# Kernel tuning notes

Measured on AMD Instinct MI355X. Metric: run time of the kernel, lower is better.

The kernel has to match this reference:

```python
import jax, jax.numpy as jnp
import numpy as np

NUM_HEADS = 32      # query heads
NUM_KV_HEADS = 8    # GQA kv heads
HEAD_DIM = 128
BS = 16             # decode batch (one new token per sequence)
KV_LEN = 2048       # pages (page_size=1 -> tokens) per sequence
NUM_SLOTS = BS * KV_LEN
SCALE = HEAD_DIM ** -0.5


def setup_inputs() -> dict:
    key = jax.random.key(0)
    ks = jax.random.split(key, 6)
    q = jax.random.normal(ks[0], (BS, NUM_HEADS * HEAD_DIM), dtype=jnp.float32)
    k = jax.random.normal(ks[1], (BS, NUM_KV_HEADS * HEAD_DIM), dtype=jnp.float32)
    v = jax.random.normal(ks[2], (BS, NUM_KV_HEADS * HEAD_DIM), dtype=jnp.float32)
    k_cache = jax.random.normal(ks[3], (NUM_SLOTS, NUM_KV_HEADS * HEAD_DIM), dtype=jnp.float32)
    v_cache = jax.random.normal(ks[4], (NUM_SLOTS, NUM_KV_HEADS * HEAD_DIM), dtype=jnp.float32)
    # paged layout: each sequence owns KV_LEN non-contiguous slots (page_size=1)
    perm = jax.random.permutation(ks[5], NUM_SLOTS).astype(jnp.int32)
    page_indices = perm.reshape(BS, KV_LEN)            # [BS, KV_LEN] slot ids
    slot_mapping = page_indices[:, -1]                 # new token written to last page
    return {"q": q, "k": k, "v": v, "k_cache": k_cache, "v_cache": v_cache,
            "slot_mapping": slot_mapping, "page_indices": page_indices}


def reference(q, k, v, k_cache, v_cache, slot_mapping, page_indices):
    # store_kvcache: scatter new K/V rows into flat [num_slots, Hkv*d] caches
    k_cache = k_cache.at[slot_mapping].set(k)
    v_cache = v_cache.at[slot_mapping].set(v)
    # paged gather (page_size=1): [BS, KV_LEN, Hkv, d]
    keys = k_cache[page_indices].reshape(BS, KV_LEN, NUM_KV_HEADS, HEAD_DIM)
    vals = v_cache[page_indices].reshape(BS, KV_LEN, NUM_KV_HEADS, HEAD_DIM)
    # GQA: query head h uses kv head h // group
    group = NUM_HEADS // NUM_KV_HEADS
    qh = q.reshape(BS, NUM_KV_HEADS, group, HEAD_DIM)
    scores = jnp.einsum('bhgd,blhd->bhgl', qh, keys) * SCALE   # [BS,Hkv,g,L]
    p = jax.nn.softmax(scores, axis=-1)
    o = jnp.einsum('bhgl,blhd->bhgd', p, vals)                 # [BS,Hkv,g,d]
    return o.reshape(BS, NUM_HEADS * HEAD_DIM)
```

## Files before the change

### kernel.cpp

```cpp
#include <hip/hip_runtime.h>
#include <math.h>

constexpr int NUM_HEADS    = 32;
constexpr int NUM_KV_HEADS = 8;
constexpr int HEAD_DIM     = 128;
constexpr int BS           = 16;
constexpr int KV_LEN       = 2048;
constexpr int GROUP        = NUM_HEADS / NUM_KV_HEADS;
constexpr int NCHUNK       = 16;
constexpr int CHUNK        = KV_LEN / NCHUNK;
constexpr int NIT          = CHUNK / 16;

__device__ __forceinline__ void dma16(const float* g, float* l) {
    __builtin_amdgcn_global_load_lds(
        (const __attribute__((address_space(1))) void*)g,
        (__attribute__((address_space(3))) void*)l,
        16, 0, 0);
}

__global__ __launch_bounds__(256, 4) void attn_partial_kernel(
    const float* __restrict__ q,
    const float* __restrict__ knew,
    const float* __restrict__ vnew,
    const float* __restrict__ k_cache,
    const float* __restrict__ v_cache,
    const int*   __restrict__ page_indices,
    float* __restrict__ ws_o,
    float* __restrict__ ws_m,
    float* __restrict__ ws_s)
{
    const int bid   = blockIdx.x;
    const int chunk = bid % NCHUNK;
    const int h     = (bid / NCHUNK) % NUM_KV_HEADS;
    const int b     = bid / (NCHUNK * NUM_KV_HEADS);

    const int tid  = threadIdx.x;
    const int wid  = tid >> 6;
    const int lane = tid & 63;
    const int g    = lane >> 4;
    const int sub  = lane & 15;
    const int lg   = wid * 4 + g;

    const int lbase = chunk * CHUNK;

    __shared__ float smem[2][4][1024];

    const float qscale = 0.08838834764831845f * 1.4426950408889634f;

    float qv[GROUP][8];
#pragma unroll
    for (int hg = 0; hg < GROUP; ++hg) {
        const float* qp = q + ((size_t)b * NUM_HEADS + h * GROUP + hg) * HEAD_DIM;
        const float4 a = *(const float4*)(qp + sub * 4);
        const float4 c = *(const float4*)(qp + 64 + sub * 4);
        qv[hg][0] = a.x * qscale; qv[hg][1] = a.y * qscale;
        qv[hg][2] = a.z * qscale; qv[hg][3] = a.w * qscale;
        qv[hg][4] = c.x * qscale; qv[hg][5] = c.y * qscale;
        qv[hg][6] = c.z * qscale; qv[hg][7] = c.w * qscale;
    }

    float m[GROUP], ssum[GROUP], o[GROUP][8];
#pragma unroll
    for (int hg = 0; hg < GROUP; ++hg) {
        m[hg] = -INFINITY; ssum[hg] = 0.f;
#pragma unroll
        for (int j = 0; j < 8; ++j) o[hg][j] = 0.f;
    }

    const float* knew_row = knew + ((size_t)b * NUM_KV_HEADS + h) * HEAD_DIM;
    const float* vnew_row = vnew + ((size_t)b * NUM_KV_HEADS + h) * HEAD_DIM;

    auto stage = [&](int buf, int l, int idx) {
        const float *kr, *vr;
        if (l == KV_LEN - 1) {
            kr = knew_row; vr = vnew_row;
        } else {
            kr = k_cache + ((size_t)idx * NUM_KV_HEADS + h) * HEAD_DIM;
            vr = v_cache + ((size_t)idx * NUM_KV_HEADS + h) * HEAD_DIM;
        }
        float* base = &smem[buf][wid][0];
        dma16(kr + sub * 4,       base);
        dma16(kr + 64 + sub * 4,  base + 256);
        dma16(vr + sub * 4,       base + 512);
        dma16(vr + 64 + sub * 4,  base + 768);
    };

    int idx_cur = page_indices[b * KV_LEN + lbase + lg];
    stage(0, lbase + lg, idx_cur);
    int idx_next = page_indices[b * KV_LEN + lbase + ((NIT > 1) ? 16 : 0) + lg];

#pragma unroll 1
    for (int t = 0; t < NIT; ++t) {
        __syncthreads();

        if (t + 1 < NIT) {
            stage((t + 1) & 1, lbase + (t + 1) * 16 + lg, idx_next);
            if (t + 2 < NIT)
                idx_next = page_indices[b * KV_LEN + lbase + (t + 2) * 16 + lg];
        }

        const float* basep = &smem[t & 1][wid][0];
        const float4 k0 = *(const float4*)(basep + g * 64 + sub * 4);
        const float4 k1 = *(const float4*)(basep + 256 + g * 64 + sub * 4);
        const float4 v0 = *(const float4*)(basep + 512 + g * 64 + sub * 4);
        const float4 v1 = *(const float4*)(basep + 768 + g * 64 + sub * 4);

        float sc[GROUP];
#pragma unroll
        for (int hg = 0; hg < GROUP; ++hg) {
            sc[hg] = qv[hg][0] * k0.x + qv[hg][1] * k0.y + qv[hg][2] * k0.z + qv[hg][3] * k0.w
                   + qv[hg][4] * k1.x + qv[hg][5] * k1.y + qv[hg][6] * k1.z + qv[hg][7] * k1.w;
        }
#pragma unroll
        for (int off = 1; off < 16; off <<= 1) {
#pragma unroll
            for (int hg = 0; hg < GROUP; ++hg)
                sc[hg] += __shfl_xor(sc[hg], off, 64);
        }
#pragma unroll
        for (int hg = 0; hg < GROUP; ++hg) {
            const float mn = fmaxf(m[hg], sc[hg]);
            const float cf = exp2f(m[hg] - mn);
            const float pr = exp2f(sc[hg] - mn);
            ssum[hg] = ssum[hg] * cf + pr;
            m[hg] = mn;
            o[hg][0] = o[hg][0] * cf + pr * v0.x;
            o[hg][1] = o[hg][1] * cf + pr * v0.y;
            o[hg][2] = o[hg][2] * cf + pr * v0.z;
            o[hg][3] = o[hg][3] * cf + pr * v0.w;
            o[hg][4] = o[hg][4] * cf + pr * v1.x;
            o[hg][5] = o[hg][5] * cf + pr * v1.y;
            o[hg][6] = o[hg][6] * cf + pr * v1.z;
            o[hg][7] = o[hg][7] * cf + pr * v1.w;
        }
    }

#pragma unroll
    for (int off = 16; off <= 32; off <<= 1) {
#pragma unroll
        for (int hg = 0; hg < GROUP; ++hg) {
            const float mo = __shfl_xor(m[hg], off, 64);
            const float so = __shfl_xor(ssum[hg], off, 64);
            float oo[8];
#pragma unroll
            for (int j = 0; j < 8; ++j) oo[j] = __shfl_xor(o[hg][j], off, 64);
            const float mn = fmaxf(m[hg], mo);
            const float c1 = exp2f(m[hg] - mn);
            const float c2 = exp2f(mo - mn);
            ssum[hg] = ssum[hg] * c1 + so * c2;
#pragma unroll
            for (int j = 0; j < 8; ++j) o[hg][j] = o[hg][j] * c1 + oo[j] * c2;
            m[hg] = mn;
        }
    }

    __syncthreads();
    float* red   = &smem[0][0][0];
    float* red_o = red;
    float* red_m = red + 2048;
    float* red_s = red + 2048 + 16;
    if (lane < 16) {
#pragma unroll
        for (int hg = 0; hg < GROUP; ++hg) {
            *(float4*)&red_o[(wid * GROUP + hg) * HEAD_DIM + sub * 4] =
                make_float4(o[hg][0], o[hg][1], o[hg][2], o[hg][3]);
            *(float4*)&red_o[(wid * GROUP + hg) * HEAD_DIM + 64 + sub * 4] =
                make_float4(o[hg][4], o[hg][5], o[hg][6], o[hg][7]);
        }
        if (sub == 0) {
#pragma unroll
            for (int hg = 0; hg < GROUP; ++hg) {
                red_m[wid * GROUP + hg] = m[hg];
                red_s[wid * GROUP + hg] = ssum[hg];
            }
        }
    }
    __syncthreads();

    if (wid == 0) {
        const int hg = g;
        const float mn = fmaxf(fmaxf(red_m[0 * GROUP + hg], red_m[1 * GROUP + hg]),
                               fmaxf(red_m[2 * GROUP + hg], red_m[3 * GROUP + hg]));
        float stot = 0.f;
        float acc[8] = {0.f,0.f,0.f,0.f,0.f,0.f,0.f,0.f};
#pragma unroll
        for (int w = 0; w < 4; ++w) {
            const float c = exp2f(red_m[w * GROUP + hg] - mn);
            stot += red_s[w * GROUP + hg] * c;
            const float* ro = &red_o[(w * GROUP + hg) * HEAD_DIM];
#pragma unroll
            for (int j = 0; j < 4; ++j) acc[j]     += ro[sub * 4 + j] * c;
#pragma unroll
            for (int j = 0; j < 4; ++j) acc[4 + j] += ro[64 + sub * 4 + j] * c;
        }
        const size_t pbase = (((size_t)chunk * BS + b) * NUM_KV_HEADS + h) * GROUP + hg;
        float* op = ws_o + pbase * HEAD_DIM;
        *(float4*)(op + sub * 4)      = make_float4(acc[0], acc[1], acc[2], acc[3]);
        *(float4*)(op + 64 + sub * 4) = make_float4(acc[4], acc[5], acc[6], acc[7]);
        if (sub == 0) { ws_m[pbase] = mn; ws_s[pbase] = stot; }
    }
}

__global__ __launch_bounds__(128) void attn_combine_kernel(
    const float* __restrict__ ws_o,
    const float* __restrict__ ws_m,
    const float* __restrict__ ws_s,
    float* __restrict__ out)
{
    const int bid = blockIdx.x;
    const int hg  = bid % GROUP;
    const int h   = (bid / GROUP) % NUM_KV_HEADS;
    const int b   = bid / (GROUP * NUM_KV_HEADS);
    const int d   = threadIdx.x;

    float mv[NCHUNK];
    float mx = -INFINITY;
#pragma unroll
    for (int c = 0; c < NCHUNK; ++c) {
        mv[c] = ws_m[(((size_t)c * BS + b) * NUM_KV_HEADS + h) * GROUP + hg];
        mx = fmaxf(mx, mv[c]);
    }
    float stot = 0.f, acc = 0.f;
#pragma unroll
    for (int c = 0; c < NCHUNK; ++c) {
        const size_t pbase = (((size_t)c * BS + b) * NUM_KV_HEADS + h) * GROUP + hg;
        const float cf = exp2f(mv[c] - mx);
        stot += ws_s[pbase] * cf;
        acc  += ws_o[pbase * HEAD_DIM + d] * cf;
    }
    out[((size_t)b * NUM_HEADS + h * GROUP + hg) * HEAD_DIM + d] = acc / stot;
}

extern "C" void kernel_launch(void* const* d_in, const int* in_sizes, int n_in,
                              void* d_out, int out_size, void* d_ws, size_t ws_size,
                              hipStream_t stream)
{
    const float* q       = (const float*)d_in[0];
    const float* k       = (const float*)d_in[1];
    const float* v       = (const float*)d_in[2];
    const float* k_cache = (const float*)d_in[3];
    const float* v_cache = (const float*)d_in[4];
    const int* page_indices = (const int*)d_in[6];
    float* out = (float*)d_out;

    float* ws_o = (float*)d_ws;
    float* ws_m = ws_o + (size_t)NCHUNK * BS * NUM_KV_HEADS * GROUP * HEAD_DIM;
    float* ws_s = ws_m + (size_t)NCHUNK * BS * NUM_KV_HEADS * GROUP;

    attn_partial_kernel<<<BS * NUM_KV_HEADS * NCHUNK, 256, 0, stream>>>(
        q, k, v, k_cache, v_cache, page_indices, ws_o, ws_m, ws_s);
    attn_combine_kernel<<<BS * NUM_KV_HEADS * GROUP, 128, 0, stream>>>(
        ws_o, ws_m, ws_s, out);
}
```

Before: 58.30 us.

## Replace block barriers with per-wave vmcnt waits and prefetch all page indices

Removes the per-iteration __syncthreads and relies on per-wave s_waitcnt vmcnt counts to wait for the LDS DMA loads. Since each wave only reads its own LDS slice, a block-wide barrier is not needed. All page indices for the chunk are loaded into registers up front, and the loop is fully unrolled with two stages kept in flight, refilling a buffer after it has been consumed. Launch bounds drop to 3 blocks per CU to leave room for the extra registers. The risk is that correctness depends on hand-written waitcnt values matching the DMA instruction count, and the extra registers may lower occupancy.

Result: slower. 79.04 us (+35.6%).

```diff
diff --git a/kernel.cpp b/kernel.cpp
--- a/kernel.cpp
+++ b/kernel.cpp
@@ -14,11 +14,10 @@
 __device__ __forceinline__ void dma16(const float* g, float* l) {
     __builtin_amdgcn_global_load_lds(
         (const __attribute__((address_space(1))) void*)g,
-        (__attribute__((address_space(3))) void*)l,
-        16, 0, 0);
-}
-
-__global__ __launch_bounds__(256, 4) void attn_partial_kernel(
+        (__attribute__((address_space(3))) void*)l, 16, 0, 0);
+}
+
+__global__ __launch_bounds__(256, 3) void attn_partial_kernel(
     const float* __restrict__ q,
     const float* __restrict__ knew,
     const float* __restrict__ vnew,
@@ -70,7 +69,13 @@
     const float* knew_row = knew + ((size_t)b * NUM_KV_HEADS + h) * HEAD_DIM;
     const float* vnew_row = vnew + ((size_t)b * NUM_KV_HEADS + h) * HEAD_DIM;
 
-    auto stage = [&](int buf, int l, int idx) {
+    int idxr[NIT];
+#pragma unroll
+    for (int t = 0; t < NIT; ++t)
+        idxr[t] = page_indices[b * KV_LEN + lbase + t * 16 + lg];
+
+    auto stage = [&](int buf, int t, int idx) {
+        const int l = lbase + t * 16 + lg;
         const float *kr, *vr;
         if (l == KV_LEN - 1) {
             kr = knew_row; vr = vnew_row;
@@ -85,25 +90,23 @@
         dma16(vr + 64 + sub * 4,  base + 768);
     };
 
-    int idx_cur = page_indices[b * KV_LEN + lbase + lg];
-    stage(0, lbase + lg, idx_cur);
-    int idx_next = page_indices[b * KV_LEN + lbase + ((NIT > 1) ? 16 : 0) + lg];
-
-#pragma unroll 1
+    stage(0, 0, idxr[0]);
+    stage(1, 1, idxr[1]);
+
+#pragma unroll
     for (int t = 0; t < NIT; ++t) {
-        __syncthreads();
-
         if (t + 1 < NIT) {
-            stage((t + 1) & 1, lbase + (t + 1) * 16 + lg, idx_next);
-            if (t + 2 < NIT)
-                idx_next = page_indices[b * KV_LEN + lbase + (t + 2) * 16 + lg];
-        }
-
-        const float* basep = &smem[t & 1][wid][0];
-        const float4 k0 = *(const float4*)(basep + g * 64 + sub * 4);
-        const float4 k1 = *(const float4*)(basep + 256 + g * 64 + sub * 4);
-        const float4 v0 = *(const float4*)(basep + 512 + g * 64 + sub * 4);
-        const float4 v1 = *(const float4*)(basep + 768 + g * 64 + sub * 4);
+            asm volatile("s_waitcnt vmcnt(4)" ::: "memory");
+        } else {
+            asm volatile("s_waitcnt vmcnt(0)" ::: "memory");
+        }
+        __builtin_amdgcn_sched_barrier(0);
+
+        const float* bp = &smem[t & 1][wid][0];
+        const float4 k0 = *(const float4*)(bp + g * 64 + sub * 4);
+        const float4 k1 = *(const float4*)(bp + 256 + g * 64 + sub * 4);
+        const float4 v0 = *(const float4*)(bp + 512 + g * 64 + sub * 4);
+        const float4 v1 = *(const float4*)(bp + 768 + g * 64 + sub * 4);
 
         float sc[GROUP];
 #pragma unroll
@@ -133,6 +136,11 @@
             o[hg][6] = o[hg][6] * cf + pr * v1.z;
             o[hg][7] = o[hg][7] * cf + pr * v1.w;
         }
+
+        if (t + 2 < NIT) {
+            asm volatile("s_waitcnt lgkmcnt(0)" ::: "memory");
+            stage(t & 1, t + 2, idxr[t + 2]);
+        }
     }
 
 #pragma unroll
```
